# Kernel tuning notes

Hardware: AMD Instinct MI355X
Metric: run time of the kernel (lower is better)

## Reference

```python
import jax, jax.numpy as jnp
import numpy as np

IN_DIMS = 32
HID = 64
N_HIDDEN = 5  # tcnn n_hidden_layers = hidden_layers + 1 = 5
OUT_DIMS = 3
BATCH = 2097152


def setup_inputs() -> dict:
    key = jax.random.key(0)
    ks = jax.random.split(key, N_HIDDEN + 2)
    x = jax.random.normal(ks[0], (BATCH, IN_DIMS), dtype=jnp.float32)
    # tcnn FullyFusedMLP has no biases; Kaiming-ish init scale
    W0 = jax.random.normal(ks[1], (IN_DIMS, HID), dtype=jnp.float32) * (1.0 / np.sqrt(IN_DIMS))
    Wh = jax.random.normal(ks[2], (N_HIDDEN - 1, HID, HID), dtype=jnp.float32) * (1.0 / np.sqrt(HID))
    Wo = jax.random.normal(ks[3], (HID, OUT_DIMS), dtype=jnp.float32) * (1.0 / np.sqrt(HID))
    return {"x": x, "W0": W0, "Wh": Wh, "Wo": Wo}


def reference(x, W0, Wh, Wo):
    # input layer -> ReLU
    h = jax.nn.relu(x @ W0)  # [B, 64]
    # 4 more hidden layers of 64->64 with ReLU (small fixed count, unrolled)
    for i in range(Wh.shape[0]):
        h = jax.nn.relu(h @ Wh[i])
    # linear output layer (output_activation = None)
    return h @ Wo  # [B, 3]
```

## Files before the change

kernel.cpp:

```cpp
#include <hip/hip_runtime.h>


typedef __attribute__((ext_vector_type(8))) short short8;
typedef __attribute__((ext_vector_type(4))) float f32x4;

#define BATCH   2097152
#define NBLOCKS 1024
#define WAVES   (NBLOCKS * 4)
#define ITERS   (BATCH / (WAVES * 16))
#define RSTRIDE 144
#define BUFSZ   (16 * RSTRIDE)
#define WREGION (2 * BUFSZ)
static_assert(BATCH == NBLOCKS * 4 * 16 * ITERS, "");

__device__ __forceinline__ unsigned cvt_pk(float a, float b) {
    unsigned r;
    asm("v_cvt_pk_bf16_f32 %0, %1, %2" : "=v"(r) : "v"(a), "v"(b));
    return r;
}

__global__ __launch_bounds__(256, 2)
void mlp_fused(const float* __restrict__ x, const float* __restrict__ W0,
               const float* __restrict__ Wh, const float* __restrict__ Wo,
               float* __restrict__ out)
{
    __shared__ __align__(16) unsigned char smem[4 * WREGION];

    const int tid  = threadIdx.x;
    const int w    = tid >> 6;
    const int lane = tid & 63;
    const int n = lane & 15;
    const int q = lane >> 4;

    short8 wf0[4], wfh[4][4][2], wfo[2];
    #pragma unroll
    for (int t = 0; t < 4; ++t) {
        const float* p = W0 + (8 * q) * 64 + 16 * t + n;
        union { unsigned u[4]; short8 s; } f;
        #pragma unroll
        for (int i = 0; i < 4; ++i)
            f.u[i] = cvt_pk(p[(2 * i) * 64], p[(2 * i + 1) * 64]);
        wf0[t] = f.s;
    }
    #pragma unroll
    for (int l = 0; l < 4; ++l)
        #pragma unroll
        for (int t = 0; t < 4; ++t)
            #pragma unroll
            for (int c = 0; c < 2; ++c) {
                const float* p = Wh + l * 4096 + (32 * c + 8 * q) * 64 + 16 * t + n;
                union { unsigned u[4]; short8 s; } f;
                #pragma unroll
                for (int i = 0; i < 4; ++i)
                    f.u[i] = cvt_pk(p[(2 * i) * 64], p[(2 * i + 1) * 64]);
                wfh[l][t][c] = f.s;
            }
    #pragma unroll
    for (int c = 0; c < 2; ++c) {
        union { unsigned u[4]; short8 s; } f;
        #pragma unroll
        for (int i = 0; i < 4; ++i) {
            float a = (n < 3) ? Wo[(32 * c + 8 * q + 2 * i)     * 3 + n] : 0.f;
            float b = (n < 3) ? Wo[(32 * c + 8 * q + 2 * i + 1) * 3 + n] : 0.f;
            f.u[i] = cvt_pk(a, b);
        }
        wfo[c] = f.s;
    }

    unsigned char* const smw = smem + w * WREGION;
    const unsigned aw = (unsigned)n * RSTRIDE + 8u  * (unsigned)q;
    const unsigned ar = (unsigned)n * RSTRIDE + 16u * (unsigned)q;

    const int gw = blockIdx.x * 4 + w;
    const f32x4 z = {0.f, 0.f, 0.f, 0.f};

    short8 xfn;
    {
        const f32x4* xp = (const f32x4*)(x + ((size_t)gw * 16 + n) * 32) + 2 * q;
        f32x4 a = xp[0], b = xp[1];
        union { unsigned u[4]; short8 s; } f;
        f.u[0] = cvt_pk(a[0], a[1]); f.u[1] = cvt_pk(a[2], a[3]);
        f.u[2] = cvt_pk(b[0], b[1]); f.u[3] = cvt_pk(b[2], b[3]);
        xfn = f.s;
    }

    #pragma unroll 1
    for (int it = 0; it < ITERS; ++it) {
        const short8 xf   = xfn;
        const size_t row0 = ((size_t)it * WAVES + gw) * 16;

        f32x4 acc[4];
        #pragma unroll
        for (int t = 0; t < 4; ++t)
            acc[t] = __builtin_amdgcn_mfma_f32_16x16x32_bf16(wf0[t], xf, z, 0, 0, 0);

        if (it + 1 < ITERS) {
            const size_t r1 = ((size_t)(it + 1) * WAVES + gw) * 16;
            const f32x4* xp = (const f32x4*)(x + (r1 + n) * 32) + 2 * q;
            f32x4 a = xp[0], b = xp[1];
            union { unsigned u[4]; short8 s; } f;
            f.u[0] = cvt_pk(a[0], a[1]); f.u[1] = cvt_pk(a[2], a[3]);
            f.u[2] = cvt_pk(b[0], b[1]); f.u[3] = cvt_pk(b[2], b[3]);
            xfn = f.s;
        }

        #pragma unroll
        for (int s = 0; s < 5; ++s) {
            unsigned char* buf = smw + (((unsigned)(s + it) & 1u) * BUFSZ);

            #pragma unroll
            for (int t = 0; t < 2; ++t) {
                uint2 wv;
                wv.x = cvt_pk(fmaxf(acc[t][0], 0.f), fmaxf(acc[t][1], 0.f));
                wv.y = cvt_pk(fmaxf(acc[t][2], 0.f), fmaxf(acc[t][3], 0.f));
                *(uint2*)(buf + aw + 32u * t) = wv;
            }
            short8 b0 = *(const short8*)(buf + ar);
            #pragma unroll
            for (int t = 2; t < 4; ++t) {
                uint2 wv;
                wv.x = cvt_pk(fmaxf(acc[t][0], 0.f), fmaxf(acc[t][1], 0.f));
                wv.y = cvt_pk(fmaxf(acc[t][2], 0.f), fmaxf(acc[t][3], 0.f));
                *(uint2*)(buf + aw + 32u * t) = wv;
            }
            short8 b1 = *(const short8*)(buf + ar + 64u);

            if (s < 4) {
                #pragma unroll
                for (int t = 0; t < 4; ++t)
                    acc[t] = __builtin_amdgcn_mfma_f32_16x16x32_bf16(
                                 wfh[s][t][0], b0, z, 0, 0, 0);
                #pragma unroll
                for (int t = 0; t < 4; ++t)
                    acc[t] = __builtin_amdgcn_mfma_f32_16x16x32_bf16(
                                 wfh[s][t][1], b1, acc[t], 0, 0, 0);
            } else {
                f32x4 o = __builtin_amdgcn_mfma_f32_16x16x32_bf16(wfo[0], b0, z, 0, 0, 0);
                o = __builtin_amdgcn_mfma_f32_16x16x32_bf16(wfo[1], b1, o, 0, 0, 0);
                if (lane < 16) {
                    float* po = out + (row0 + lane) * 3;
                    po[0] = o[0]; po[1] = o[1]; po[2] = o[2];
                }
            }
        }
    }
}

extern "C" void kernel_launch(void* const* d_in, const int* in_sizes, int n_in,
                              void* d_out, int out_size, void* d_ws, size_t ws_size,
                              hipStream_t stream) {
    (void)in_sizes; (void)n_in; (void)d_ws; (void)ws_size; (void)out_size;
    const float* x  = (const float*)d_in[0];
    const float* W0 = (const float*)d_in[1];
    const float* Wh = (const float*)d_in[2];
    const float* Wo = (const float*)d_in[3];
    float* out = (float*)d_out;
    mlp_fused<<<NBLOCKS, 256, 0, stream>>>(x, W0, Wh, Wo, out);
}
```

Before: 402.2 us.

## Process two independent 16-row tiles per wave to interleave MFMA chains

After: 386.0 us. -4.0%, faster.

```diff
diff --git a/kernel.cpp b/kernel.cpp
--- a/kernel.cpp
+++ b/kernel.cpp
@@ -7,11 +7,11 @@
 #define BATCH   2097152
 #define NBLOCKS 1024
 #define WAVES   (NBLOCKS * 4)
-#define ITERS   (BATCH / (WAVES * 16))
+#define ROWS_PW 32
+#define ITERS   (BATCH / (WAVES * ROWS_PW))
 #define RSTRIDE 144
 #define BUFSZ   (16 * RSTRIDE)
-#define WREGION (2 * BUFSZ)
-static_assert(BATCH == NBLOCKS * 4 * 16 * ITERS, "");
+static_assert(BATCH == (size_t)WAVES * ROWS_PW * ITERS, "");
 
 __device__ __forceinline__ unsigned cvt_pk(float a, float b) {
     unsigned r;
@@ -24,7 +24,7 @@
                const float* __restrict__ Wh, const float* __restrict__ Wo,
                float* __restrict__ out)
 {
-    __shared__ __align__(16) unsigned char smem[4 * WREGION];
+    __shared__ __align__(16) unsigned char smem[4 * 2 * BUFSZ];
 
     const int tid  = threadIdx.x;
     const int w    = tid >> 6;
@@ -67,80 +67,97 @@
         wfo[c] = f.s;
     }
 
-    unsigned char* const smw = smem + w * WREGION;
+    unsigned char* const bufA = smem + w * (2 * BUFSZ);
+    unsigned char* const bufB = bufA + BUFSZ;
     const unsigned aw = (unsigned)n * RSTRIDE + 8u  * (unsigned)q;
     const unsigned ar = (unsigned)n * RSTRIDE + 16u * (unsigned)q;
 
     const int gw = blockIdx.x * 4 + w;
     const f32x4 z = {0.f, 0.f, 0.f, 0.f};
 
-    short8 xfn;
-    {
-        const f32x4* xp = (const f32x4*)(x + ((size_t)gw * 16 + n) * 32) + 2 * q;
-        f32x4 a = xp[0], b = xp[1];
+    f32x4 rawA[2], rawB[2];
+    auto issue_x = [&](int it) {
+        const size_t r = ((size_t)it * WAVES + gw) * ROWS_PW;
+        const f32x4* pA = (const f32x4*)(x + (r + n) * 32) + 2 * q;
+        rawA[0] = pA[0]; rawA[1] = pA[1];
+        const f32x4* pB = (const f32x4*)(x + (r + 16 + n) * 32) + 2 * q;
+        rawB[0] = pB[0]; rawB[1] = pB[1];
+    };
+    auto convert_x = [&](const f32x4* raw) -> short8 {
         union { unsigned u[4]; short8 s; } f;
-        f.u[0] = cvt_pk(a[0], a[1]); f.u[1] = cvt_pk(a[2], a[3]);
-        f.u[2] = cvt_pk(b[0], b[1]); f.u[3] = cvt_pk(b[2], b[3]);
-        xfn = f.s;
-    }
+        f.u[0] = cvt_pk(raw[0][0], raw[0][1]);
+        f.u[1] = cvt_pk(raw[0][2], raw[0][3]);
+        f.u[2] = cvt_pk(raw[1][0], raw[1][1]);
+        f.u[3] = cvt_pk(raw[1][2], raw[1][3]);
+        return f.s;
+    };
+    auto stage = [&](const f32x4 (&acc)[4], unsigned char* buf,
+                     short8& b0, short8& b1) {
+        #pragma unroll
+        for (int t = 0; t < 4; ++t) {
+            uint2 wv;
+            wv.x = cvt_pk(fmaxf(acc[t][0], 0.f), fmaxf(acc[t][1], 0.f));
+            wv.y = cvt_pk(fmaxf(acc[t][2], 0.f), fmaxf(acc[t][3], 0.f));
+            *(uint2*)(buf + aw + 32u * t) = wv;
+        }
+        b0 = *(const short8*)(buf + ar);
+        b1 = *(const short8*)(buf + ar + 64u);
+    };
+
+    issue_x(0);
 
     #pragma unroll 1
     for (int it = 0; it < ITERS; ++it) {
-        const short8 xf   = xfn;
-        const size_t row0 = ((size_t)it * WAVES + gw) * 16;
+        const short8 xfA = convert_x(rawA);
+        const short8 xfB = convert_x(rawB);
+        if (it + 1 < ITERS) issue_x(it + 1);
 
-        f32x4 acc[4];
+        const size_t row0 = ((size_t)it * WAVES + gw) * ROWS_PW;
+
+        f32x4 accA[4], accB[4];
         #pragma unroll
         for (int t = 0; t < 4; ++t)
-            acc[t] = __builtin_amdgcn_mfma_f32_16x16x32_bf16(wf0[t], xf, z, 0, 0, 0);
+            accA[t] = __builtin_amdgcn_mfma_f32_16x16x32_bf16(wf0[t], xfA, z, 0, 0, 0);
+        #pragma unroll
+        for (int t = 0; t < 4; ++t)
+            accB[t] = __builtin_amdgcn_mfma_f32_16x16x32_bf16(wf0[t], xfB, z, 0, 0, 0);
 
-        if (it + 1 < ITERS) {
-            const size_t r1 = ((size_t)(it + 1) * WAVES + gw) * 16;
-            const f32x4* xp = (const f32x4*)(x + (r1 + n) * 32) + 2 * q;
-            f32x4 a = xp[0], b = xp[1];
-            union { unsigned u[4]; short8 s; } f;
-            f.u[0] = cvt_pk(a[0], a[1]); f.u[1] = cvt_pk(a[2], a[3]);
-            f.u[2] = cvt_pk(b[0], b[1]); f.u[3] = cvt_pk(b[2], b[3]);
-            xfn = f.s;
+        #pragma unroll
+        for (int s = 0; s < 4; ++s) {
+            short8 a0, a1, c0, c1;
+            stage(accA, bufA, a0, a1);
+            stage(accB, bufB, c0, c1);
+            #pragma unroll
+            for (int t = 0; t < 4; ++t)
+                accA[t] = __builtin_amdgcn_mfma_f32_16x16x32_bf16(
+                              wfh[s][t][0], a0, z, 0, 0, 0);
+            #pragma unroll
+            for (int t = 0; t < 4; ++t)
+                accA[t] = __builtin_amdgcn_mfma_f32_16x16x32_bf16(
+                              wfh[s][t][1], a1, accA[t], 0, 0, 0);
+            #pragma unroll
+            for (int t = 0; t < 4; ++t)
+                accB[t] = __builtin_amdgcn_mfma_f32_16x16x32_bf16(
+                              wfh[s][t][0], c0, z, 0, 0, 0);
+            #pragma unroll
+            for (int t = 0; t < 4; ++t)
+                accB[t] = __builtin_amdgcn_mfma_f32_16x16x32_bf16(
+                              wfh[s][t][1], c1, accB[t], 0, 0, 0);
         }
 
-        #pragma unroll
-        for (int s = 0; s < 5; ++s) {
-            unsigned char* buf = smw + (((unsigned)(s + it) & 1u) * BUFSZ);
-
-            #pragma unroll
-            for (int t = 0; t < 2; ++t) {
-                uint2 wv;
-                wv.x = cvt_pk(fmaxf(acc[t][0], 0.f), fmaxf(acc[t][1], 0.f));
-                wv.y = cvt_pk(fmaxf(acc[t][2], 0.f), fmaxf(acc[t][3], 0.f));
-                *(uint2*)(buf + aw + 32u * t) = wv;
-            }
-            short8 b0 = *(const short8*)(buf + ar);
-            #pragma unroll
-            for (int t = 2; t < 4; ++t) {
-                uint2 wv;
-                wv.x = cvt_pk(fmaxf(acc[t][0], 0.f), fmaxf(acc[t][1], 0.f));
-                wv.y = cvt_pk(fmaxf(acc[t][2], 0.f), fmaxf(acc[t][3], 0.f));
-                *(uint2*)(buf + aw + 32u * t) = wv;
-            }
-            short8 b1 = *(const short8*)(buf + ar + 64u);
-
-            if (s < 4) {
-                #pragma unroll
-                for (int t = 0; t < 4; ++t)
-                    acc[t] = __builtin_amdgcn_mfma_f32_16x16x32_bf16(
-                                 wfh[s][t][0], b0, z, 0, 0, 0);
-                #pragma unroll
-                for (int t = 0; t < 4; ++t)
-                    acc[t] = __builtin_amdgcn_mfma_f32_16x16x32_bf16(
-                                 wfh[s][t][1], b1, acc[t], 0, 0, 0);
-            } else {
-                f32x4 o = __builtin_amdgcn_mfma_f32_16x16x32_bf16(wfo[0], b0, z, 0, 0, 0);
-                o = __builtin_amdgcn_mfma_f32_16x16x32_bf16(wfo[1], b1, o, 0, 0, 0);
-                if (lane < 16) {
-                    float* po = out + (row0 + lane) * 3;
-                    po[0] = o[0]; po[1] = o[1]; po[2] = o[2];
-                }
+        {
+            short8 a0, a1, c0, c1;
+            stage(accA, bufA, a0, a1);
+            stage(accB, bufB, c0, c1);
+            f32x4 oA = __builtin_amdgcn_mfma_f32_16x16x32_bf16(wfo[0], a0, z, 0, 0, 0);
+            oA = __builtin_amdgcn_mfma_f32_16x16x32_bf16(wfo[1], a1, oA, 0, 0, 0);
+            f32x4 oB = __builtin_amdgcn_mfma_f32_16x16x32_bf16(wfo[0], c0, z, 0, 0, 0);
+            oB = __builtin_amdgcn_mfma_f32_16x16x32_bf16(wfo[1], c1, oB, 0, 0, 0);
+            if (lane < 16) {
+                float* pA = out + (row0 + lane) * 3;
+                pA[0] = oA[0]; pA[1] = oA[1]; pA[2] = oA[2];
+                float* pB = out + (row0 + 16 + lane) * 3;
+                pB[0] = oB[0]; pB[1] = oB[1]; pB[2] = oB[2];
             }
         }
     }
```
